# Performance work log

Measured on AMD Instinct MI355X. Metric: run time of the kernel, lower is better.

Reference implementation:

```python
import jax, jax.numpy as jnp
import numpy as np

N = 50000          # num nodes
DEG = 16           # fixed degree (uniform CSR)
E = N * DEG        # num edges
R = 8              # num relations
IN = 128
HID = 128
OUT = 40
BN_EPS = 1e-5


def setup_inputs() -> dict:
    key = jax.random.key(0)
    k = jax.random.split(key, 5)
    x = jax.random.normal(k[0], (N, IN), jnp.float32)
    # glorot-ish init for per-relation weights
    W1 = jax.random.normal(k[1], (R, IN, HID), jnp.float32) * (2.0 / (IN + HID)) ** 0.5
    W2 = jax.random.normal(k[2], (R, HID, OUT), jnp.float32) * (2.0 / (HID + OUT)) ** 0.5
    ptr = jnp.arange(N + 1, dtype=jnp.int32) * DEG            # CSR row offsets
    idx = jax.random.randint(k[3], (E,), 0, N, jnp.int32)     # neighbor (src) ids
    edge_types = jax.random.randint(k[4], (E,), 0, R, jnp.int32)
    return {
        "x": x, "W1": W1, "W2": W2,
        "bn_gamma": jnp.ones((HID,), jnp.float32),
        "bn_beta": jnp.zeros((HID,), jnp.float32),
        "bn_mean": jnp.zeros((HID,), jnp.float32),
        "bn_var": jnp.ones((HID,), jnp.float32),
        "ptr": ptr, "idx": idx, "edge_types": edge_types,
    }


def _rgcn_layer(h, W, ptr, idx, edge_types):
    # RGCNOP: out[i] = sum_{e in [ptr[i],ptr[i+1])} x[idx[e]] @ W[etype[e]]
    # Efficient form: transform every node by every relation once, then gather
    # the (src, etype) pair per edge and scatter-add into destinations.
    xr = jnp.einsum('nd,rdh->nrh', h, W)             # [N, R, H]
    msgs = xr[idx, edge_types]                       # [E, H] irregular gather
    deg = ptr[1:] - ptr[:-1]                         # [N]
    dst = jnp.repeat(jnp.arange(ptr.shape[0] - 1, dtype=jnp.int32), deg,
                     total_repeat_length=idx.shape[0])
    agg = jax.ops.segment_sum(msgs, dst, num_segments=ptr.shape[0] - 1)
    return agg / deg[:, None].astype(agg.dtype)      # degree normalization


def reference(x, W1, W2, bn_gamma, bn_beta, bn_mean, bn_var, ptr, idx, edge_types):
    h = _rgcn_layer(x, W1, ptr, idx, edge_types)
    # BatchNorm1d in eval mode (history_size=0, dropout inactive)
    h = (h - bn_mean) * jax.lax.rsqrt(bn_var + BN_EPS) * bn_gamma + bn_beta
    h = jax.nn.relu(h)
    h = _rgcn_layer(h, W2, ptr, idx, edge_types)
    return jax.nn.log_softmax(h, axis=-1)
```

## Files before the change

kernel.cpp:

```cpp
#include <hip/hip_runtime.h>
#include <math.h>

typedef __attribute__((ext_vector_type(8))) short bf16x8;
typedef __attribute__((ext_vector_type(4))) float f32x4;

constexpr int kN   = 50000;
constexpr int kR   = 8;
constexpr int kIn  = 128;
constexpr int kHid = 128;
constexpr int kOut = 40;
constexpr int kNT  = 16;
constexpr int kLds = 1032;
constexpr float kBnEps = 1e-5f;

__device__ inline ushort f2bf(float x) {
    uint u = __float_as_uint(x);
    u += 0x7FFFu + ((u >> 16) & 1u);
    return (ushort)(u >> 16);
}
__device__ inline float bf2f(ushort s) { return __uint_as_float(((uint)s) << 16); }

__device__ __forceinline__ void pack_unit(const float* __restrict__ W,
                                          ushort* __restrict__ dst,
                                          int N, int frag, int lane)
{
    const int kt = frag & 31;
    const int nt = frag >> 5;
    const int n  = nt * 16 + (lane & 15);
    const int q  = lane >> 4;
    ushort hv[8];
    #pragma unroll
    for (int j = 0; j < 8; ++j) {
        const int k = kt * 32 + q * 8 + j;
        hv[j] = f2bf((n < N) ? W[(size_t)k * N + n] : 0.f);
    }
    const size_t o = ((size_t)frag * 64 + lane) * 8;
    *(ushort4*)&dst[o]     = make_ushort4(hv[0], hv[1], hv[2], hv[3]);
    *(ushort4*)&dst[o + 4] = make_ushort4(hv[4], hv[5], hv[6], hv[7]);
}

__global__ __launch_bounds__(256)
void prep(const float* __restrict__ x,  ushort* __restrict__ xb,
          const float* __restrict__ W1, ushort* __restrict__ W1hi,
          const float* __restrict__ W2, ushort* __restrict__ W2hi)
{
    const int b   = blockIdx.x;
    const int tid = threadIdx.x;
    if (b < 3125) {
        const size_t i = ((size_t)b * 256 + tid) * 8;
        const float4 v0 = *(const float4*)&x[i];
        const float4 v1 = *(const float4*)&x[i + 4];
        *(ushort4*)&xb[i]     = make_ushort4(f2bf(v0.x), f2bf(v0.y), f2bf(v0.z), f2bf(v0.w));
        *(ushort4*)&xb[i + 4] = make_ushort4(f2bf(v1.x), f2bf(v1.y), f2bf(v1.z), f2bf(v1.w));
    } else if (b < 3125 + 64) {
        pack_unit(W1, W1hi, kHid, (b - 3125) * 4 + (tid >> 6), tid & 63);
    } else {
        const int frag = (b - 3189) * 4 + (tid >> 6);
        if (frag < 96) pack_unit(W2, W2hi, kOut, frag, tid & 63);
    }
}

#define ACCUM_ET(ET, VX, VY)                                   \
    if      ((ET) == 0) { a0.x += (VX); a0.y += (VY); }        \
    else if ((ET) == 1) { a1.x += (VX); a1.y += (VY); }        \
    else if ((ET) == 2) { a2.x += (VX); a2.y += (VY); }        \
    else if ((ET) == 3) { a3.x += (VX); a3.y += (VY); }        \
    else if ((ET) == 4) { a4.x += (VX); a4.y += (VY); }        \
    else if ((ET) == 5) { a5.x += (VX); a5.y += (VY); }        \
    else if ((ET) == 6) { a6.x += (VX); a6.y += (VY); }        \
    else                { a7.x += (VX); a7.y += (VY); }

#define GATHER(BV, SRC) \
    const ushort2 BV = *(const ushort2*)&feat[(size_t)(SRC) * 128 + d2];

#define ACCUM_EDGE(J, BV) \
    { const int et = __builtin_amdgcn_readlane(ve, J); ACCUM_ET(et, bf2f(BV.x), bf2f(BV.y)) }

#define STORE_AGG(RR, AV) \
    *(ushort2*)&aggHi[n][(RR) * 128 + d2] = make_ushort2(f2bf(AV.x), f2bf(AV.y));

__device__ __forceinline__ void phaseA_bf16(const ushort* __restrict__ feat,
                                            const int* __restrict__ ptr,
                                            const int* __restrict__ idx,
                                            const int* __restrict__ etype,
                                            int base, ushort (*aggHi)[kLds])
{
    const int lane = threadIdx.x & 63;
    const int wid  = threadIdx.x >> 6;
    const int d2   = lane * 2;

    #pragma unroll
    for (int t = 0; t < 2; ++t) {
        const int n    = wid * 2 + t;
        const int node = base + n;
        const int p0   = ptr[node];
        const int deg  = ptr[node + 1] - p0;

        float2 a0 = {0.f,0.f}, a1 = {0.f,0.f}, a2 = {0.f,0.f}, a3 = {0.f,0.f};
        float2 a4 = {0.f,0.f}, a5 = {0.f,0.f}, a6 = {0.f,0.f}, a7 = {0.f,0.f};

        if (deg == 16) {
            const int vi = idx[p0 + (lane & 15)];
            const int ve = etype[p0 + (lane & 15)];
            const int s0  = __builtin_amdgcn_readlane(vi, 0);
            const int s1  = __builtin_amdgcn_readlane(vi, 1);
            const int s2  = __builtin_amdgcn_readlane(vi, 2);
            const int s3  = __builtin_amdgcn_readlane(vi, 3);
            const int s4  = __builtin_amdgcn_readlane(vi, 4);
            const int s5  = __builtin_amdgcn_readlane(vi, 5);
            const int s6  = __builtin_amdgcn_readlane(vi, 6);
            const int s7  = __builtin_amdgcn_readlane(vi, 7);
            const int s8  = __builtin_amdgcn_readlane(vi, 8);
            const int s9  = __builtin_amdgcn_readlane(vi, 9);
            const int s10 = __builtin_amdgcn_readlane(vi, 10);
            const int s11 = __builtin_amdgcn_readlane(vi, 11);
            const int s12 = __builtin_amdgcn_readlane(vi, 12);
            const int s13 = __builtin_amdgcn_readlane(vi, 13);
            const int s14 = __builtin_amdgcn_readlane(vi, 14);
            const int s15 = __builtin_amdgcn_readlane(vi, 15);
            GATHER(b0,  s0)  GATHER(b1,  s1)  GATHER(b2,  s2)  GATHER(b3,  s3)
            GATHER(b4,  s4)  GATHER(b5,  s5)  GATHER(b6,  s6)  GATHER(b7,  s7)
            GATHER(b8,  s8)  GATHER(b9,  s9)  GATHER(b10, s10) GATHER(b11, s11)
            GATHER(b12, s12) GATHER(b13, s13) GATHER(b14, s14) GATHER(b15, s15)
            ACCUM_EDGE(0,  b0)  ACCUM_EDGE(1,  b1)  ACCUM_EDGE(2,  b2)  ACCUM_EDGE(3,  b3)
            ACCUM_EDGE(4,  b4)  ACCUM_EDGE(5,  b5)  ACCUM_EDGE(6,  b6)  ACCUM_EDGE(7,  b7)
            ACCUM_EDGE(8,  b8)  ACCUM_EDGE(9,  b9)  ACCUM_EDGE(10, b10) ACCUM_EDGE(11, b11)
            ACCUM_EDGE(12, b12) ACCUM_EDGE(13, b13) ACCUM_EDGE(14, b14) ACCUM_EDGE(15, b15)
        } else {
            for (int e = p0; e < p0 + deg; ++e) {
                const int src = __builtin_amdgcn_readfirstlane(idx[e]);
                const int et  = __builtin_amdgcn_readfirstlane(etype[e]);
                const ushort2 u = *(const ushort2*)&feat[(size_t)src * 128 + d2];
                ACCUM_ET(et, bf2f(u.x), bf2f(u.y))
            }
        }
        STORE_AGG(0, a0) STORE_AGG(1, a1) STORE_AGG(2, a2) STORE_AGG(3, a3)
        STORE_AGG(4, a4) STORE_AGG(5, a5) STORE_AGG(6, a6) STORE_AGG(7, a7)
    }
}

__global__ __launch_bounds__(512, 4)
void rgcn_layer1(const ushort* __restrict__ xb,
                 const ushort* __restrict__ W1hi,
                 const float* __restrict__ gamma, const float* __restrict__ beta,
                 const float* __restrict__ mean,  const float* __restrict__ var,
                 const int* __restrict__ ptr, const int* __restrict__ idx,
                 const int* __restrict__ etype,
                 ushort* __restrict__ h1b)
{
    __shared__ ushort aggHi[kNT][kLds];
    const int tid  = threadIdx.x;
    const int base = blockIdx.x * kNT;

    phaseA_bf16(xb, ptr, idx, etype, base, aggHi);
    __syncthreads();

    const int lane = tid & 63;
    const int wid  = tid >> 6;
    const int m    = lane & 15;
    const int q    = lane >> 4;

    const bf16x8* Bh = (const bf16x8*)W1hi + (size_t)wid * 32 * 64 + lane;
    f32x4 acc = {0.f, 0.f, 0.f, 0.f};

    #pragma unroll 4
    for (int kt = 0; kt < 32; ++kt) {
        const bf16x8 ah = *(const bf16x8*)&aggHi[m][kt * 32 + q * 8];
        const bf16x8 bh = Bh[(size_t)kt * 64];
        acc = __builtin_amdgcn_mfma_f32_16x16x32_bf16(ah, bh, acc, 0, 0, 0);
    }

    const int c = wid * 16 + m;
    const float g  = gamma[c] * rsqrtf(var[c] + kBnEps);
    const float mu = mean[c];
    const float bt = beta[c];
    #pragma unroll
    for (int i = 0; i < 4; ++i) {
        const int node = base + q * 4 + i;
        const float invdeg = 1.0f / (float)(ptr[node + 1] - ptr[node]);
        float v = (acc[i] * invdeg - mu) * g + bt;
        v = fmaxf(v, 0.f);
        h1b[(size_t)node * kHid + c] = f2bf(v);
    }
}

__global__ __launch_bounds__(512, 4)
void rgcn_layer2(const ushort* __restrict__ h1b,
                 const ushort* __restrict__ W2hi,
                 const int* __restrict__ ptr, const int* __restrict__ idx,
                 const int* __restrict__ etype,
                 float* __restrict__ out)
{
    __shared__ ushort aggHi[kNT][kLds];
    __shared__ float logits[kNT][48];
    const int tid  = threadIdx.x;
    const int base = blockIdx.x * kNT;

    phaseA_bf16(h1b, ptr, idx, etype, base, aggHi);
    __syncthreads();

    const int lane = tid & 63;
    const int wid  = tid >> 6;
    const int m    = lane & 15;
    const int q    = lane >> 4;

    if (wid < 3) {
        const bf16x8* Bh = (const bf16x8*)W2hi + (size_t)wid * 32 * 64 + lane;
        f32x4 acc = {0.f, 0.f, 0.f, 0.f};
        #pragma unroll 4
        for (int kt = 0; kt < 32; ++kt) {
            const bf16x8 ah = *(const bf16x8*)&aggHi[m][kt * 32 + q * 8];
            const bf16x8 bh = Bh[(size_t)kt * 64];
            acc = __builtin_amdgcn_mfma_f32_16x16x32_bf16(ah, bh, acc, 0, 0, 0);
        }
        const int n = wid * 16 + m;
        if (n < kOut) {
            #pragma unroll
            for (int i = 0; i < 4; ++i) {
                const int node = base + q * 4 + i;
                const float invdeg = 1.0f / (float)(ptr[node + 1] - ptr[node]);
                logits[q * 4 + i][n] = acc[i] * invdeg;
            }
        }
    }
    __syncthreads();

    #pragma unroll
    for (int i = 0; i < 2; ++i) {
        const int nrow = wid * 2 + i;
        const int node = base + nrow;
        const float v = (lane < kOut) ? logits[nrow][lane] : -INFINITY;
        float mx = v;
        #pragma unroll
        for (int off = 32; off > 0; off >>= 1)
            mx = fmaxf(mx, __shfl_xor(mx, off, 64));
        float s = (lane < kOut) ? __expf(v - mx) : 0.f;
        #pragma unroll
        for (int off = 32; off > 0; off >>= 1)
            s += __shfl_xor(s, off, 64);
        if (lane < kOut)
            out[(size_t)node * kOut + lane] = v - mx - __logf(s);
    }
}

extern "C" void kernel_launch(void* const* d_in, const int* in_sizes, int n_in,
                              void* d_out, int out_size, void* d_ws, size_t ws_size,
                              hipStream_t stream)
{
    const float* x     = (const float*)d_in[0];
    const float* W1    = (const float*)d_in[1];
    const float* W2    = (const float*)d_in[2];
    const float* gamma = (const float*)d_in[3];
    const float* beta  = (const float*)d_in[4];
    const float* mean  = (const float*)d_in[5];
    const float* var   = (const float*)d_in[6];
    const int*   ptr   = (const int*)d_in[7];
    const int*   idx   = (const int*)d_in[8];
    const int*   et    = (const int*)d_in[9];
    float*       out   = (float*)d_out;

    char* ws = (char*)d_ws;
    ushort* h1b  = (ushort*)ws;
    ushort* xb   = (ushort*)(ws + 12800000);
    ushort* W1hi = (ushort*)(ws + 25600000);
    ushort* W2hi = (ushort*)(ws + 25600000 + 262144);

    prep<<<dim3(3125 + 64 + 24), dim3(256), 0, stream>>>(x, xb, W1, W1hi, W2, W2hi);

    dim3 grid(kN / kNT), block(512);
    rgcn_layer1<<<grid, block, 0, stream>>>(xb, W1hi, gamma, beta, mean, var,
                                            ptr, idx, et, h1b);
    rgcn_layer2<<<grid, block, 0, stream>>>(h1b, W2hi, ptr, idx, et, out);
}
```

Measured before the change: 194.1 us.

## Precompute per-relation node transforms then gather-aggregate instead of fused per-edge matmul

Adds a path that first transforms every node by all relations with MFMA GEMMs into a bf16 buffer of shape N×R×H. Separate per-node kernels then gather the (src, etype) rows, applying batchnorm+ReLU for layer 1 and log-softmax for layer 2. This replaces the old fused per-destination kernels, which presumably did the per-edge matmul work inside the aggregation. In exchange it writes and randomly reads a ~100MB intermediate and needs a large workspace, with fallback to the old path if the workspace is too small.

```diff
diff --git a/kernel.cpp b/kernel.cpp
--- a/kernel.cpp
+++ b/kernel.cpp
@@ -19,6 +19,278 @@
     return (ushort)(u >> 16);
 }
 __device__ inline float bf2f(ushort s) { return __uint_as_float(((uint)s) << 16); }
+__device__ inline ushort f2bf_c(float x) {
+    return (ushort)((__float_as_uint(x) + 0x8000u) >> 16);
+}
+
+
+__global__ __launch_bounds__(256)
+void prep_new(const float* __restrict__ x,  ushort* __restrict__ xb,
+              const float* __restrict__ W1, ushort* __restrict__ W1p,
+              const float* __restrict__ W2, ushort* __restrict__ W2p)
+{
+    const int b   = blockIdx.x;
+    const int tid = threadIdx.x;
+    if (b < 3125) {
+        const size_t i = ((size_t)b * 256 + tid) * 8;
+        const float4 v0 = *(const float4*)&x[i];
+        const float4 v1 = *(const float4*)&x[i + 4];
+        *(ushort4*)&xb[i]     = make_ushort4(f2bf(v0.x), f2bf(v0.y), f2bf(v0.z), f2bf(v0.w));
+        *(ushort4*)&xb[i + 4] = make_ushort4(f2bf(v1.x), f2bf(v1.y), f2bf(v1.z), f2bf(v1.w));
+        return;
+    }
+    const int lane = tid & 63;
+    const int m = lane & 15, q = lane >> 4;
+    ushort hv[8];
+    if (b < 3125 + 64) {
+        const int f  = (b - 3125) * 4 + (tid >> 6);
+        const int nt = f >> 2, kt = f & 3;
+        const int n  = nt * 16 + m;
+        const int r  = n >> 7, h = n & 127;
+        #pragma unroll
+        for (int j = 0; j < 8; ++j) {
+            const int k = kt * 32 + q * 8 + j;
+            hv[j] = f2bf(W1[(size_t)r * 16384 + (size_t)k * 128 + h]);
+        }
+        const size_t o = ((size_t)f * 64 + lane) * 8;
+        *(ushort4*)&W1p[o]     = make_ushort4(hv[0], hv[1], hv[2], hv[3]);
+        *(ushort4*)&W1p[o + 4] = make_ushort4(hv[4], hv[5], hv[6], hv[7]);
+    } else {
+        const int f  = (b - 3189) * 4 + (tid >> 6);
+        const int nt = f >> 2, kt = f & 3;
+        const int n  = nt * 16 + m;
+        const int r  = n >> 6, h = n & 63;
+        #pragma unroll
+        for (int j = 0; j < 8; ++j) {
+            const int k = kt * 32 + q * 8 + j;
+            hv[j] = (h < kOut) ? f2bf(W2[(size_t)r * 5120 + (size_t)k * 40 + h])
+                               : (ushort)0;
+        }
+        const size_t o = ((size_t)f * 64 + lane) * 8;
+        *(ushort4*)&W2p[o]     = make_ushort4(hv[0], hv[1], hv[2], hv[3]);
+        *(ushort4*)&W2p[o + 4] = make_ushort4(hv[4], hv[5], hv[6], hv[7]);
+    }
+}
+
+#define LOADA(MT,KT) const bf16x8 af##MT##KT = \
+    *(const bf16x8*)&As[MT * 16 + m][KT * 32 + q * 8];
+
+template<int NTW, int NCOLS>
+__global__ __launch_bounds__(512, 4)
+void xform(const ushort* __restrict__ in,
+           const ushort* __restrict__ Bp,
+           ushort* __restrict__ outp)
+{
+    __shared__ ushort As[64][136];
+    const int tid  = threadIdx.x;
+    const int base = blockIdx.x * 64;
+
+    {
+        const int row = tid >> 3, c = tid & 7;
+        const int gr  = base + row;
+        bf16x8 v0 = {0,0,0,0,0,0,0,0}, v1 = {0,0,0,0,0,0,0,0};
+        if (gr < kN) {
+            v0 = *(const bf16x8*)&in[(size_t)gr * 128 + c * 8];
+            v1 = *(const bf16x8*)&in[(size_t)gr * 128 + c * 8 + 64];
+        }
+        *(bf16x8*)&As[row][c * 8]      = v0;
+        *(bf16x8*)&As[row][c * 8 + 64] = v1;
+    }
+    __syncthreads();
+
+    const int lane = tid & 63, wid = tid >> 6;
+    const int m = lane & 15, q = lane >> 4;
+
+    LOADA(0,0) LOADA(0,1) LOADA(0,2) LOADA(0,3)
+    LOADA(1,0) LOADA(1,1) LOADA(1,2) LOADA(1,3)
+    LOADA(2,0) LOADA(2,1) LOADA(2,2) LOADA(2,3)
+    LOADA(3,0) LOADA(3,1) LOADA(3,2) LOADA(3,3)
+
+    const bf16x8* B8 = (const bf16x8*)Bp;
+
+    #pragma unroll
+    for (int ii = 0; ii < NTW; ++ii) {
+        const int nt = wid * NTW + ii;
+        const bf16x8 b0 = B8[(size_t)(nt * 4 + 0) * 64 + lane];
+        const bf16x8 b1 = B8[(size_t)(nt * 4 + 1) * 64 + lane];
+        const bf16x8 b2 = B8[(size_t)(nt * 4 + 2) * 64 + lane];
+        const bf16x8 b3 = B8[(size_t)(nt * 4 + 3) * 64 + lane];
+        f32x4 c0 = {0.f,0.f,0.f,0.f}, c1 = {0.f,0.f,0.f,0.f};
+        f32x4 c2 = {0.f,0.f,0.f,0.f}, c3 = {0.f,0.f,0.f,0.f};
+        c0 = __builtin_amdgcn_mfma_f32_16x16x32_bf16(af00, b0, c0, 0, 0, 0);
+        c1 = __builtin_amdgcn_mfma_f32_16x16x32_bf16(af10, b0, c1, 0, 0, 0);
+        c2 = __builtin_amdgcn_mfma_f32_16x16x32_bf16(af20, b0, c2, 0, 0, 0);
+        c3 = __builtin_amdgcn_mfma_f32_16x16x32_bf16(af30, b0, c3, 0, 0, 0);
+        c0 = __builtin_amdgcn_mfma_f32_16x16x32_bf16(af01, b1, c0, 0, 0, 0);
+        c1 = __builtin_amdgcn_mfma_f32_16x16x32_bf16(af11, b1, c1, 0, 0, 0);
+        c2 = __builtin_amdgcn_mfma_f32_16x16x32_bf16(af21, b1, c2, 0, 0, 0);
+        c3 = __builtin_amdgcn_mfma_f32_16x16x32_bf16(af31, b1, c3, 0, 0, 0);
+        c0 = __builtin_amdgcn_mfma_f32_16x16x32_bf16(af02, b2, c0, 0, 0, 0);
+        c1 = __builtin_amdgcn_mfma_f32_16x16x32_bf16(af12, b2, c1, 0, 0, 0);
+        c2 = __builtin_amdgcn_mfma_f32_16x16x32_bf16(af22, b2, c2, 0, 0, 0);
+        c3 = __builtin_amdgcn_mfma_f32_16x16x32_bf16(af32, b2, c3, 0, 0, 0);
+        c0 = __builtin_amdgcn_mfma_f32_16x16x32_bf16(af03, b3, c0, 0, 0, 0);
+        c1 = __builtin_amdgcn_mfma_f32_16x16x32_bf16(af13, b3, c1, 0, 0, 0);
+        c2 = __builtin_amdgcn_mfma_f32_16x16x32_bf16(af23, b3, c2, 0, 0, 0);
+        c3 = __builtin_amdgcn_mfma_f32_16x16x32_bf16(af33, b3, c3, 0, 0, 0);
+
+        const int col = nt * 16 + m;
+        #define STORE_MT(CC, MT) {                                          \
+            const int r0 = base + MT * 16 + q * 4;                          \
+            _Pragma("unroll")                                               \
+            for (int i2 = 0; i2 < 4; ++i2) {                                \
+                const int rr = r0 + i2;                                     \
+                if (rr < kN)                                                \
+                    outp[(size_t)rr * NCOLS + col] = f2bf_c(CC[i2]);        \
+            } }
+        STORE_MT(c0, 0) STORE_MT(c1, 1) STORE_MT(c2, 2) STORE_MT(c3, 3)
+        #undef STORE_MT
+    }
+}
+
+#define GADD(BV, GJ) \
+    const uint BV = xrU[(size_t)(GJ) * 64 + lane]; \
+    ax += __uint_as_float((BV) << 16); \
+    ay += __uint_as_float((BV) & 0xffff0000u);
+
+__global__ __launch_bounds__(512, 4)
+void agg_bn(const ushort* __restrict__ xr1,
+            const int* __restrict__ ptr, const int* __restrict__ idx,
+            const int* __restrict__ etype,
+            const float* __restrict__ gamma, const float* __restrict__ beta,
+            const float* __restrict__ mean,  const float* __restrict__ var,
+            ushort* __restrict__ h1b)
+{
+    const int lane = threadIdx.x & 63;
+    const int wid  = threadIdx.x >> 6;
+    const int node = blockIdx.x * 8 + wid;
+    const int p0 = ptr[node], p1 = ptr[node + 1];
+    const int deg = p1 - p0;
+    const uint* xrU = (const uint*)xr1;
+
+    float ax = 0.f, ay = 0.f;
+    if (deg == 16) {
+        const int gv = (idx[p0 + (lane & 15)] << 3) | etype[p0 + (lane & 15)];
+        const int g0  = __builtin_amdgcn_readlane(gv, 0);
+        const int g1  = __builtin_amdgcn_readlane(gv, 1);
+        const int g2  = __builtin_amdgcn_readlane(gv, 2);
+        const int g3  = __builtin_amdgcn_readlane(gv, 3);
+        const int g4  = __builtin_amdgcn_readlane(gv, 4);
+        const int g5  = __builtin_amdgcn_readlane(gv, 5);
+        const int g6  = __builtin_amdgcn_readlane(gv, 6);
+        const int g7  = __builtin_amdgcn_readlane(gv, 7);
+        const int g8  = __builtin_amdgcn_readlane(gv, 8);
+        const int g9  = __builtin_amdgcn_readlane(gv, 9);
+        const int g10 = __builtin_amdgcn_readlane(gv, 10);
+        const int g11 = __builtin_amdgcn_readlane(gv, 11);
+        const int g12 = __builtin_amdgcn_readlane(gv, 12);
+        const int g13 = __builtin_amdgcn_readlane(gv, 13);
+        const int g14 = __builtin_amdgcn_readlane(gv, 14);
+        const int g15 = __builtin_amdgcn_readlane(gv, 15);
+        GADD(b0,  g0)  GADD(b1,  g1)  GADD(b2,  g2)  GADD(b3,  g3)
+        GADD(b4,  g4)  GADD(b5,  g5)  GADD(b6,  g6)  GADD(b7,  g7)
+        GADD(b8,  g8)  GADD(b9,  g9)  GADD(b10, g10) GADD(b11, g11)
+        GADD(b12, g12) GADD(b13, g13) GADD(b14, g14) GADD(b15, g15)
+    } else {
+        for (int e = p0; e < p1; ++e) {
+            const int src = __builtin_amdgcn_readfirstlane(idx[e]);
+            const int et  = __builtin_amdgcn_readfirstlane(etype[e]);
+            const uint b  = xrU[((size_t)src * 8 + et) * 64 + lane];
+            ax += __uint_as_float(b << 16);
+            ay += __uint_as_float(b & 0xffff0000u);
+        }
+    }
+
+    const float invd = 1.0f / (float)deg;
+    const int c0 = lane * 2;
+    const float2 gm = *(const float2*)&gamma[c0];
+    const float2 bt = *(const float2*)&beta[c0];
+    const float2 mu = *(const float2*)&mean[c0];
+    const float2 vr = *(const float2*)&var[c0];
+    float v0 = (ax * invd - mu.x) * (gm.x * rsqrtf(vr.x + kBnEps)) + bt.x;
+    float v1 = (ay * invd - mu.y) * (gm.y * rsqrtf(vr.y + kBnEps)) + bt.y;
+    v0 = fmaxf(v0, 0.f);
+    v1 = fmaxf(v1, 0.f);
+    const uint px = (__float_as_uint(v0) + 0x8000u) >> 16;
+    const uint py = (__float_as_uint(v1) + 0x8000u) & 0xffff0000u;
+    ((uint*)h1b)[(size_t)node * 64 + lane] = px | py;
+}
+
+#define GADD2(BV, GJ) \
+    const uint BV = xrU[(size_t)(GJ) * 32 + lane]; \
+    ax += __uint_as_float((BV) << 16); \
+    ay += __uint_as_float((BV) & 0xffff0000u);
+
+__global__ __launch_bounds__(512, 4)
+void agg_sm(const ushort* __restrict__ xr2,
+            const int* __restrict__ ptr, const int* __restrict__ idx,
+            const int* __restrict__ etype,
+            float* __restrict__ out)
+{
+    const int lane = threadIdx.x & 63;
+    const int wid  = threadIdx.x >> 6;
+    const int node = blockIdx.x * 8 + wid;
+    const int p0 = ptr[node], p1 = ptr[node + 1];
+    const int deg = p1 - p0;
+    const uint* xrU = (const uint*)xr2;
+
+    float ax = 0.f, ay = 0.f;
+    if (deg == 16) {
+        const int gv = (idx[p0 + (lane & 15)] << 3) | etype[p0 + (lane & 15)];
+        const int g0  = __builtin_amdgcn_readlane(gv, 0);
+        const int g1  = __builtin_amdgcn_readlane(gv, 1);
+        const int g2  = __builtin_amdgcn_readlane(gv, 2);
+        const int g3  = __builtin_amdgcn_readlane(gv, 3);
+        const int g4  = __builtin_amdgcn_readlane(gv, 4);
+        const int g5  = __builtin_amdgcn_readlane(gv, 5);
+        const int g6  = __builtin_amdgcn_readlane(gv, 6);
+        const int g7  = __builtin_amdgcn_readlane(gv, 7);
+        const int g8  = __builtin_amdgcn_readlane(gv, 8);
+        const int g9  = __builtin_amdgcn_readlane(gv, 9);
+        const int g10 = __builtin_amdgcn_readlane(gv, 10);
+        const int g11 = __builtin_amdgcn_readlane(gv, 11);
+        const int g12 = __builtin_amdgcn_readlane(gv, 12);
+        const int g13 = __builtin_amdgcn_readlane(gv, 13);
+        const int g14 = __builtin_amdgcn_readlane(gv, 14);
+        const int g15 = __builtin_amdgcn_readlane(gv, 15);
+        if (lane < 20) {
+            GADD2(b0,  g0)  GADD2(b1,  g1)  GADD2(b2,  g2)  GADD2(b3,  g3)
+            GADD2(b4,  g4)  GADD2(b5,  g5)  GADD2(b6,  g6)  GADD2(b7,  g7)
+            GADD2(b8,  g8)  GADD2(b9,  g9)  GADD2(b10, g10) GADD2(b11, g11)
+            GADD2(b12, g12) GADD2(b13, g13) GADD2(b14, g14) GADD2(b15, g15)
+        }
+    } else {
+        for (int e = p0; e < p1; ++e) {
+            const int src = __builtin_amdgcn_readfirstlane(idx[e]);
+            const int et  = __builtin_amdgcn_readfirstlane(etype[e]);
+            if (lane < 20) {
+                const uint b = xrU[((size_t)src * 8 + et) * 32 + lane];
+                ax += __uint_as_float(b << 16);
+                ay += __uint_as_float(b & 0xffff0000u);
+            }
+        }
+    }
+
+    const float invd = 1.0f / (float)deg;
+    ax *= invd; ay *= invd;
+
+    float mx = (lane < 20) ? fmaxf(ax, ay) : -INFINITY;
+    #pragma unroll
+    for (int off = 32; off > 0; off >>= 1)
+        mx = fmaxf(mx, __shfl_xor(mx, off, 64));
+    float s = (lane < 20) ? (__expf(ax - mx) + __expf(ay - mx)) : 0.f;
+    #pragma unroll
+    for (int off = 32; off > 0; off >>= 1)
+        s += __shfl_xor(s, off, 64);
+    const float ls = __logf(s);
+    if (lane < 20) {
+        float2 o;
+        o.x = ax - mx - ls;
+        o.y = ay - mx - ls;
+        *(float2*)&out[(size_t)node * kOut + lane * 2] = o;
+    }
+}
+
 
 __device__ __forceinline__ void pack_unit(const float* __restrict__ W,
                                           ushort* __restrict__ dst,
@@ -40,9 +312,9 @@
 }
 
 __global__ __launch_bounds__(256)
-void prep(const float* __restrict__ x,  ushort* __restrict__ xb,
-          const float* __restrict__ W1, ushort* __restrict__ W1hi,
-          const float* __restrict__ W2, ushort* __restrict__ W2hi)
+void prep_old(const float* __restrict__ x,  ushort* __restrict__ xb,
+              const float* __restrict__ W1, ushort* __restrict__ W1hi,
+              const float* __restrict__ W2, ushort* __restrict__ W2hi)
 {
     const int b   = blockIdx.x;
     const int tid = threadIdx.x;
@@ -260,15 +532,31 @@
     float*       out   = (float*)d_out;
 
     char* ws = (char*)d_ws;
-    ushort* h1b  = (ushort*)ws;
-    ushort* xb   = (ushort*)(ws + 12800000);
-    ushort* W1hi = (ushort*)(ws + 25600000);
-    ushort* W2hi = (ushort*)(ws + 25600000 + 262144);
-
-    prep<<<dim3(3125 + 64 + 24), dim3(256), 0, stream>>>(x, xb, W1, W1hi, W2, W2hi);
-
-    dim3 grid(kN / kNT), block(512);
-    rgcn_layer1<<<grid, block, 0, stream>>>(xb, W1hi, gamma, beta, mean, var,
-                                            ptr, idx, et, h1b);
-    rgcn_layer2<<<grid, block, 0, stream>>>(h1b, W2hi, ptr, idx, et, out);
-}
+    constexpr size_t kNeedNew = 128393216;
+
+    if (ws_size >= kNeedNew) {
+        ushort* xb  = (ushort*)ws;
+        ushort* h1b = (ushort*)(ws + 12800000);
+        ushort* W1p = (ushort*)(ws + 25600000);
+        ushort* W2p = (ushort*)(ws + 25862144);
+        ushort* xr  = (ushort*)(ws + 25993216);
+
+        prep_new<<<dim3(3125 + 64 + 32), dim3(256), 0, stream>>>(x, xb, W1, W1p, W2, W2p);
+        xform<8, 1024><<<dim3(782), dim3(512), 0, stream>>>(xb, W1p, xr);
+        agg_bn<<<dim3(6250), dim3(512), 0, stream>>>(xr, ptr, idx, et,
+                                                     gamma, beta, mean, var, h1b);
+        xform<4, 512><<<dim3(782), dim3(512), 0, stream>>>(h1b, W2p, xr);
+        agg_sm<<<dim3(6250), dim3(512), 0, stream>>>(xr, ptr, idx, et, out);
+    } else {
+        ushort* h1b  = (ushort*)ws;
+        ushort* xb   = (ushort*)(ws + 12800000);
+        ushort* W1hi = (ushort*)(ws + 25600000);
+        ushort* W2hi = (ushort*)(ws + 25600000 + 262144);
+
+        prep_old<<<dim3(3125 + 64 + 24), dim3(256), 0, stream>>>(x, xb, W1, W1hi, W2, W2hi);
+        dim3 grid(kN / kNT), block(512);
+        rgcn_layer1<<<grid, block, 0, stream>>>(xb, W1hi, gamma, beta, mean, var,
+                                                ptr, idx, et, h1b);
+        rgcn_layer2<<<grid, block, 0, stream>>>(h1b, W2hi, ptr, idx, et, out);
+    }
+}
```

Measured after the change: 212.9 us. 9.7% more time.
